# Optimization experiments

Measured on AMD Instinct MI355X. Metric: run time of the kernel, lower is better.

## Reference

```python
import jax, jax.numpy as jnp
import numpy as np

N_NODES = 100000
D_IN = 128
D_OUT = 128
N_EDGES = 50000
EDGE_SIZE = 16  # nodes per hyperedge (assumed unique within an edge)


def setup_inputs() -> dict:
    key = jax.random.key(0)
    ks = jax.random.split(key, 8)
    # hypergraph in flat membership (CSR-like) form
    member_nodes = jax.random.randint(ks[0], (N_EDGES * EDGE_SIZE,), 0, N_NODES)
    edge_ids = jnp.repeat(jnp.arange(N_EDGES), EDGE_SIZE)
    H = jax.random.normal(ks[1], (N_NODES, D_IN), dtype=jnp.float32)
    input_weight = jax.random.uniform(ks[2], (N_NODES, 2), dtype=jnp.float32)
    std = 1.0 / np.sqrt(D_OUT)
    W = jax.random.uniform(ks[3], (D_IN, D_OUT), minval=-std, maxval=std, dtype=jnp.float32)
    bias = jax.random.uniform(ks[4], (D_OUT,), minval=-std, maxval=std, dtype=jnp.float32)

    def lin(k, fan_in, fan_out):
        b = 1.0 / np.sqrt(fan_in)
        k1, k2 = jax.random.split(k)
        w = jax.random.uniform(k1, (fan_in, fan_out), minval=-b, maxval=b, dtype=jnp.float32)
        bb = jax.random.uniform(k2, (fan_out,), minval=-b, maxval=b, dtype=jnp.float32)
        return w, bb

    fc1_w, fc1_b = lin(ks[5], 2, 10)
    fc2_w, fc2_b = lin(ks[6], 10, 5)
    fc3_w, fc3_b = lin(ks[7], 5, 1)
    return {
        "member_nodes": member_nodes, "edge_ids": edge_ids,
        "H": H, "input_weight": input_weight,
        "W": W, "bias": bias,
        "fc1_w": fc1_w, "fc1_b": fc1_b,
        "fc2_w": fc2_w, "fc2_b": fc2_b,
        "fc3_w": fc3_w, "fc3_b": fc3_b,
    }


def reference(member_nodes, edge_ids, H, input_weight, W, bias,
              fc1_w, fc1_b, fc2_w, fc2_b, fc3_w, fc3_b):
    # Weight_net (eval mode -> dropout is identity): per-node scalar weight in (0,1)
    h1 = jax.nn.relu(input_weight @ fc1_w + fc1_b)
    h2 = jax.nn.relu(h1 @ fc2_w + fc2_b)
    W2 = jax.nn.sigmoid(h2 @ fc3_w + fc3_b)  # [N, 1]

    # signal_shift_hypergraph_: per-edge weighted sum, broadcast, scatter-add
    HW2 = H * W2                                   # [N, d]
    gathered = HW2[member_nodes]                   # [M, d]
    edge_sum = jax.ops.segment_sum(gathered, edge_ids, num_segments=N_EDGES)   # [E, d]
    edge_size = jax.ops.segment_sum(jnp.ones((member_nodes.shape[0],), H.dtype),
                                    edge_ids, num_segments=N_EDGES)            # [E]
    contrib = (edge_sum[edge_ids] - H[member_nodes]) / (edge_size[edge_ids] - 1.0)[:, None]
    new_signal = H + jax.ops.segment_sum(contrib, member_nodes, num_segments=N_NODES)

    # row-normalize (1/rowsum with inf -> 0)
    rowsum = new_signal.sum(axis=1)
    r_inv = jnp.where(rowsum != 0, 1.0 / rowsum, 0.0)
    AH = new_signal * r_inv[:, None]

    return AH @ W + bias
```

## Files before the change

### kernel.cpp

```cpp
#include <hip/hip_runtime.h>
#include <math.h>

#define EDGE_SZ 16
#define CAP 32

typedef __attribute__((ext_vector_type(8))) short bf16x8;
typedef __attribute__((ext_vector_type(4))) float f32x4;

__device__ __forceinline__ unsigned short f2bf(float x) {
    unsigned u = __builtin_bit_cast(unsigned, x);
    unsigned r = (u + 0x7fff + ((u >> 16) & 1)) >> 16;
    return (unsigned short)r;
}
__device__ __forceinline__ unsigned pack2bf(float lo, float hi) {
    return ((unsigned)f2bf(hi) << 16) | (unsigned)f2bf(lo);
}
__device__ __forceinline__ float bf_lo(unsigned u) {
    return __builtin_bit_cast(float, u << 16);
}
__device__ __forceinline__ float bf_hi(unsigned u) {
    return __builtin_bit_cast(float, u & 0xffff0000u);
}

__global__ __launch_bounds__(256) void prep_kernel(
    const float* __restrict__ H, const float* __restrict__ iw,
    const float* __restrict__ fc1_w, const float* __restrict__ fc1_b,
    const float* __restrict__ fc2_w, const float* __restrict__ fc2_b,
    const float* __restrict__ fc3_w, const float* __restrict__ fc3_b,
    unsigned* __restrict__ Hwb, float* __restrict__ Hs, float* __restrict__ Hws,
    int* __restrict__ cursor, int n)
{
    int wave = __builtin_amdgcn_readfirstlane(
        blockIdx.x * (blockDim.x >> 6) + (threadIdx.x >> 6));
    int lane = threadIdx.x & 63;
    if (wave >= n) return;
    float xx = iw[wave * 2 + 0], xy = iw[wave * 2 + 1];
    float h1[10];
#pragma unroll
    for (int j = 0; j < 10; ++j) {
        float v = xx * fc1_w[j] + xy * fc1_w[10 + j] + fc1_b[j];
        h1[j] = v > 0.f ? v : 0.f;
    }
    float h2[5];
#pragma unroll
    for (int j = 0; j < 5; ++j) {
        float v = fc2_b[j];
#pragma unroll
        for (int k = 0; k < 10; ++k) v += h1[k] * fc2_w[k * 5 + j];
        h2[j] = v > 0.f ? v : 0.f;
    }
    float z = fc3_b[0];
#pragma unroll
    for (int j = 0; j < 5; ++j) z += h2[j] * fc3_w[j];
    float w2v = 1.f / (1.f + expf(-z));

    float2 h = ((const float2*)H)[wave * 64 + lane];
    Hwb[wave * 64 + lane] = pack2bf(h.x * w2v, h.y * w2v);
    float part = h.x + h.y;
#pragma unroll
    for (int off = 32; off >= 1; off >>= 1) part += __shfl_xor(part, off, 64);
    if (lane == 0) { Hs[wave] = part; Hws[wave] = part * w2v; cursor[wave] = 0; }
}

__global__ __launch_bounds__(256) void wt_kernel(
    const float* __restrict__ W, unsigned short* __restrict__ Wtg)
{
    int i = blockIdx.x * blockDim.x + threadIdx.x;
    int n = i >> 7, k = i & 127;
    Wtg[i] = f2bf(W[k * 128 + n]);
}

__global__ void fill_kernel(const int* __restrict__ mn, int* __restrict__ cursor,
                            unsigned short* __restrict__ bucket, int m)
{
    int i = blockIdx.x * blockDim.x + threadIdx.x;
    if (i < m) {
        int node = mn[i];
        int pos = atomicAdd(&cursor[node], 1);
        if (pos < CAP)
            bucket[node * CAP + pos] = (unsigned short)(i >> 4);
    }
}

__global__ __launch_bounds__(256) void edge_sum_kernel(
    const int* __restrict__ mn, const unsigned* __restrict__ Hwb,
    const float* __restrict__ Hws, unsigned* __restrict__ esb,
    float* __restrict__ Se, int E)
{
    int pair = __builtin_amdgcn_readfirstlane(
        blockIdx.x * (blockDim.x >> 6) + (threadIdx.x >> 6));
    int lane = threadIdx.x & 63;
    int e0 = pair * 2;
    if (e0 >= E) return;
    int e1 = e0 + 1;
    int n0[EDGE_SZ], n1[EDGE_SZ];
#pragma unroll
    for (int m = 0; m < EDGE_SZ; ++m) n0[m] = mn[e0 * EDGE_SZ + m];
#pragma unroll
    for (int m = 0; m < EDGE_SZ; ++m) n1[m] = mn[e1 * EDGE_SZ + m];
    unsigned u0[EDGE_SZ], u1[EDGE_SZ];
#pragma unroll
    for (int m = 0; m < EDGE_SZ; ++m) u0[m] = Hwb[n0[m] * 64 + lane];
#pragma unroll
    for (int m = 0; m < EDGE_SZ; ++m) u1[m] = Hwb[n1[m] * 64 + lane];
    float se0 = 0.f, se1 = 0.f;
#pragma unroll
    for (int m = 0; m < EDGE_SZ; ++m) { se0 += Hws[n0[m]]; se1 += Hws[n1[m]]; }
    float ax0 = 0.f, ay0 = 0.f, ax1 = 0.f, ay1 = 0.f;
#pragma unroll
    for (int m = 0; m < EDGE_SZ; ++m) {
        ax0 += bf_lo(u0[m]); ay0 += bf_hi(u0[m]);
        ax1 += bf_lo(u1[m]); ay1 += bf_hi(u1[m]);
    }
    esb[e0 * 64 + lane] = pack2bf(ax0, ay0);
    esb[e1 * 64 + lane] = pack2bf(ax1, ay1);
    if (lane == 0) { Se[e0] = se0; Se[e1] = se1; }
}

__global__ __launch_bounds__(256) void node_update_kernel(
    const float* __restrict__ H, const unsigned* __restrict__ esb,
    const float* __restrict__ Hs, const float* __restrict__ Se,
    const int* __restrict__ cursor, const unsigned short* __restrict__ bucket,
    unsigned* __restrict__ AHb, int n, int E)
{
    int pair = __builtin_amdgcn_readfirstlane(
        blockIdx.x * (blockDim.x >> 6) + (threadIdx.x >> 6));
    int lane = threadIdx.x & 63;
    int n0 = pair * 2;
    if (n0 >= n) return;
    int n1 = n0 + 1;
    float2 h0 = ((const float2*)H)[n0 * 64 + lane];
    float2 h1 = ((const float2*)H)[n1 * 64 + lane];
    int d0 = cursor[n0]; if (d0 > CAP) d0 = CAP;
    int d1 = cursor[n1]; if (d1 > CAP) d1 = CAP;
    const unsigned* b0 = (const unsigned*)(bucket + (size_t)n0 * CAP);
    const unsigned* b1 = (const unsigned*)(bucket + (size_t)n1 * CAP);
    float ax0 = 0.f, ay0 = 0.f, ss0 = 0.f;
    float ax1 = 0.f, ay1 = 0.f, ss1 = 0.f;
    int dm = d0 > d1 ? d0 : d1;
    for (int k0 = 0; k0 < dm; k0 += 8) {
        int e0[8], e1[8];
#pragma unroll
        for (int j = 0; j < 8; ++j) {
            unsigned dw0 = b0[(k0 >> 1) + (j >> 1)];
            unsigned dw1 = b1[(k0 >> 1) + (j >> 1)];
            unsigned ev0 = (j & 1) ? (dw0 >> 16) : (dw0 & 0xffffu);
            unsigned ev1 = (j & 1) ? (dw1 >> 16) : (dw1 & 0xffffu);
            e0[j] = ev0 < (unsigned)E ? (int)ev0 : 0;
            e1[j] = ev1 < (unsigned)E ? (int)ev1 : 0;
        }
        unsigned v0[8], v1[8];
#pragma unroll
        for (int j = 0; j < 8; ++j) v0[j] = esb[e0[j] * 64 + lane];
#pragma unroll
        for (int j = 0; j < 8; ++j) v1[j] = esb[e1[j] * 64 + lane];
        float s0[8], s1[8];
#pragma unroll
        for (int j = 0; j < 8; ++j) { s0[j] = Se[e0[j]]; s1[j] = Se[e1[j]]; }
#pragma unroll
        for (int j = 0; j < 8; ++j) {
            bool p0 = (k0 + j < d0), p1 = (k0 + j < d1);
            ax0 += p0 ? bf_lo(v0[j]) : 0.f;
            ay0 += p0 ? bf_hi(v0[j]) : 0.f;
            ss0 += p0 ? s0[j] : 0.f;
            ax1 += p1 ? bf_lo(v1[j]) : 0.f;
            ay1 += p1 ? bf_hi(v1[j]) : 0.f;
            ss1 += p1 ? s1[j] : 0.f;
        }
    }
    const float inv15 = 1.f / 15.f;
    float sc0 = 1.f - (float)d0 * inv15;
    float sc1 = 1.f - (float)d1 * inv15;
    float nx0 = h0.x * sc0 + ax0 * inv15, ny0 = h0.y * sc0 + ay0 * inv15;
    float nx1 = h1.x * sc1 + ax1 * inv15, ny1 = h1.y * sc1 + ay1 * inv15;
    float s0t = Hs[n0] * sc0 + ss0 * inv15;
    float s1t = Hs[n1] * sc1 + ss1 * inv15;
    float ri0 = (s0t != 0.f) ? 1.f / s0t : 0.f;
    float ri1 = (s1t != 0.f) ? 1.f / s1t : 0.f;
    AHb[n0 * 64 + lane] = pack2bf(nx0 * ri0, ny0 * ri0);
    AHb[n1 * 64 + lane] = pack2bf(nx1 * ri1, ny1 * ri1);
}

#define WT_LD 136
__global__ __launch_bounds__(256) void gemm_kernel(
    const unsigned short* __restrict__ AHb, const unsigned short* __restrict__ Wtg,
    const float* __restrict__ bias, float* __restrict__ out, int M)
{
    __shared__ short Wt[128 * WT_LD];
    int t = threadIdx.x;
    for (int i = t; i < 8192; i += 256) {
        unsigned dw = ((const unsigned*)Wtg)[i];
        int n = i >> 6, k2 = i & 63;
        *(unsigned*)&Wt[n * WT_LD + k2 * 2] = dw;
    }
    __syncthreads();

    int lane = t & 63;
    int m16 = lane & 15;
    int quad = lane >> 4;
    int wrow0 = blockIdx.x * 64 + (t >> 6) * 16;

    int arow = wrow0 + m16;
    if (arow >= M) arow = M - 1;

    f32x4 acc[8] = {};
#pragma unroll
    for (int kc = 0; kc < 4; ++kc) {
        int k0 = kc * 32;
        bf16x8 a = *(const bf16x8*)&AHb[arow * 128 + k0 + quad * 8];
#pragma unroll
        for (int ct = 0; ct < 8; ++ct) {
            bf16x8 b = *(const bf16x8*)&Wt[(ct * 16 + m16) * WT_LD + k0 + quad * 8];
            acc[ct] = __builtin_amdgcn_mfma_f32_16x16x32_bf16(a, b, acc[ct], 0, 0, 0);
        }
    }

#pragma unroll
    for (int ct = 0; ct < 8; ++ct) {
        float bv = bias[ct * 16 + m16];
#pragma unroll
        for (int r = 0; r < 4; ++r) {
            int row = wrow0 + quad * 4 + r;
            if (row < M)
                out[row * 128 + ct * 16 + m16] = acc[ct][r] + bv;
        }
    }
}

extern "C" void kernel_launch(void* const* d_in, const int* in_sizes, int n_in,
                              void* d_out, int out_size, void* d_ws, size_t ws_size,
                              hipStream_t stream)
{
    const int*   mn   = (const int*)d_in[0];
    const float* H    = (const float*)d_in[2];
    const float* iw   = (const float*)d_in[3];
    const float* W    = (const float*)d_in[4];
    const float* bias = (const float*)d_in[5];
    const float* fc1w = (const float*)d_in[6];
    const float* fc1b = (const float*)d_in[7];
    const float* fc2w = (const float*)d_in[8];
    const float* fc2b = (const float*)d_in[9];
    const float* fc3w = (const float*)d_in[10];
    const float* fc3b = (const float*)d_in[11];
    float* out = (float*)d_out;

    const int M = in_sizes[0];
    const int E = M / EDGE_SZ;
    const int N = in_sizes[2] / 128;

    char* ws = (char*)d_ws;
    size_t off = 0;
    auto alloc = [&](size_t bytes) -> char* {
        char* p = ws + off;
        off = (off + bytes + 15) & ~(size_t)15;
        return p;
    };
    unsigned*       Hwb    = (unsigned*)alloc((size_t)N * 64 * 4);
    float*          Hs     = (float*)alloc((size_t)N * 4);
    float*          Hws    = (float*)alloc((size_t)N * 4);
    unsigned*       esb    = (unsigned*)alloc((size_t)E * 64 * 4);
    float*          Se     = (float*)alloc((size_t)E * 4);
    unsigned*       AHb    = (unsigned*)alloc((size_t)N * 64 * 4);
    int*            cursor = (int*)alloc((size_t)N * 4);
    unsigned short* bucket = (unsigned short*)alloc((size_t)N * CAP * 2);
    unsigned short* Wtg    = (unsigned short*)alloc((size_t)128 * 128 * 2);
    (void)ws_size;

    prep_kernel<<<(N + 3) / 4, 256, 0, stream>>>(
        H, iw, fc1w, fc1b, fc2w, fc2b, fc3w, fc3b, Hwb, Hs, Hws, cursor, N);
    wt_kernel<<<64, 256, 0, stream>>>(W, Wtg);
    fill_kernel<<<(M + 255) / 256, 256, 0, stream>>>(mn, cursor, bucket, M);
    edge_sum_kernel<<<(E / 2 + 3) / 4, 256, 0, stream>>>(mn, Hwb, Hws, esb, Se, E);
    node_update_kernel<<<(N / 2 + 3) / 4, 256, 0, stream>>>(
        H, esb, Hs, Se, cursor, bucket, AHb, N, E);
    gemm_kernel<<<(N + 63) / 64, 256, 0, stream>>>(
        (const unsigned short*)AHb, Wtg, bias, out, N);
}
```

Baseline: 278.3 us.

## Merge prep and fill kernels, move cursor reset to init, batch four nodes per wave

Folds the weight transpose and the cursor zeroing into a small init kernel. Runs the bucket fill and the per-node prep as disjoint block ranges of a single launch, which cuts the launch count and lets the two independent workloads overlap. The node update kernel now handles four nodes per wave instead of two, issuing more independent gathers per loop iteration to hide latency. The cost is more register pressure, and more lanes sit idle on padding when the nodes in a group have uneven degrees.

```diff
diff --git a/kernel.cpp b/kernel.cpp
--- a/kernel.cpp
+++ b/kernel.cpp
@@ -22,16 +22,40 @@
     return __builtin_bit_cast(float, u & 0xffff0000u);
 }
 
-__global__ __launch_bounds__(256) void prep_kernel(
+__global__ __launch_bounds__(256) void init_kernel(
+    const float* __restrict__ W, unsigned short* __restrict__ Wtg,
+    int* __restrict__ cursor, int n)
+{
+    int i = blockIdx.x * blockDim.x + threadIdx.x;
+    if (i < n) cursor[i] = 0;
+    if (i < 16384) {
+        int nn = i >> 7, k = i & 127;
+        Wtg[i] = f2bf(W[k * 128 + nn]);
+    }
+}
+
+__global__ __launch_bounds__(256) void prep_fill_kernel(
     const float* __restrict__ H, const float* __restrict__ iw,
     const float* __restrict__ fc1_w, const float* __restrict__ fc1_b,
     const float* __restrict__ fc2_w, const float* __restrict__ fc2_b,
     const float* __restrict__ fc3_w, const float* __restrict__ fc3_b,
     unsigned* __restrict__ Hwb, float* __restrict__ Hs, float* __restrict__ Hws,
-    int* __restrict__ cursor, int n)
-{
+    const int* __restrict__ mn, int* __restrict__ cursor,
+    unsigned short* __restrict__ bucket,
+    int n, int m, int fill_blocks)
+{
+    if ((int)blockIdx.x < fill_blocks) {
+        int i = blockIdx.x * blockDim.x + threadIdx.x;
+        if (i < m) {
+            int node = mn[i];
+            int pos = atomicAdd(&cursor[node], 1);
+            if (pos < CAP)
+                bucket[node * CAP + pos] = (unsigned short)(i >> 4);
+        }
+        return;
+    }
     int wave = __builtin_amdgcn_readfirstlane(
-        blockIdx.x * (blockDim.x >> 6) + (threadIdx.x >> 6));
+        (blockIdx.x - fill_blocks) * (blockDim.x >> 6) + (threadIdx.x >> 6));
     int lane = threadIdx.x & 63;
     if (wave >= n) return;
     float xx = iw[wave * 2 + 0], xy = iw[wave * 2 + 1];
@@ -59,27 +83,7 @@
     float part = h.x + h.y;
 #pragma unroll
     for (int off = 32; off >= 1; off >>= 1) part += __shfl_xor(part, off, 64);
-    if (lane == 0) { Hs[wave] = part; Hws[wave] = part * w2v; cursor[wave] = 0; }
-}
-
-__global__ __launch_bounds__(256) void wt_kernel(
-    const float* __restrict__ W, unsigned short* __restrict__ Wtg)
-{
-    int i = blockIdx.x * blockDim.x + threadIdx.x;
-    int n = i >> 7, k = i & 127;
-    Wtg[i] = f2bf(W[k * 128 + n]);
-}
-
-__global__ void fill_kernel(const int* __restrict__ mn, int* __restrict__ cursor,
-                            unsigned short* __restrict__ bucket, int m)
-{
-    int i = blockIdx.x * blockDim.x + threadIdx.x;
-    if (i < m) {
-        int node = mn[i];
-        int pos = atomicAdd(&cursor[node], 1);
-        if (pos < CAP)
-            bucket[node * CAP + pos] = (unsigned short)(i >> 4);
-    }
+    if (lane == 0) { Hs[wave] = part; Hws[wave] = part * w2v; }
 }
 
 __global__ __launch_bounds__(256) void edge_sum_kernel(
@@ -123,62 +127,69 @@
     const int* __restrict__ cursor, const unsigned short* __restrict__ bucket,
     unsigned* __restrict__ AHb, int n, int E)
 {
-    int pair = __builtin_amdgcn_readfirstlane(
+    int grp = __builtin_amdgcn_readfirstlane(
         blockIdx.x * (blockDim.x >> 6) + (threadIdx.x >> 6));
     int lane = threadIdx.x & 63;
-    int n0 = pair * 2;
-    if (n0 >= n) return;
-    int n1 = n0 + 1;
-    float2 h0 = ((const float2*)H)[n0 * 64 + lane];
-    float2 h1 = ((const float2*)H)[n1 * 64 + lane];
-    int d0 = cursor[n0]; if (d0 > CAP) d0 = CAP;
-    int d1 = cursor[n1]; if (d1 > CAP) d1 = CAP;
-    const unsigned* b0 = (const unsigned*)(bucket + (size_t)n0 * CAP);
-    const unsigned* b1 = (const unsigned*)(bucket + (size_t)n1 * CAP);
-    float ax0 = 0.f, ay0 = 0.f, ss0 = 0.f;
-    float ax1 = 0.f, ay1 = 0.f, ss1 = 0.f;
-    int dm = d0 > d1 ? d0 : d1;
+    int base = grp * 4;
+    if (base >= n) return;
+    float2 h[4];
+    int d[4];
+    const unsigned* bp[4];
+    float ax[4], ay[4], ss[4];
+    int dm = 0;
+#pragma unroll
+    for (int q = 0; q < 4; ++q) {
+        int nq = base + q; if (nq >= n) nq = n - 1;
+        h[q] = ((const float2*)H)[nq * 64 + lane];
+        int dq = cursor[nq]; if (dq > CAP) dq = CAP;
+        if (base + q >= n) dq = 0;
+        d[q] = dq;
+        if (dq > dm) dm = dq;
+        bp[q] = (const unsigned*)(bucket + (size_t)nq * CAP);
+        ax[q] = 0.f; ay[q] = 0.f; ss[q] = 0.f;
+    }
     for (int k0 = 0; k0 < dm; k0 += 8) {
-        int e0[8], e1[8];
-#pragma unroll
-        for (int j = 0; j < 8; ++j) {
-            unsigned dw0 = b0[(k0 >> 1) + (j >> 1)];
-            unsigned dw1 = b1[(k0 >> 1) + (j >> 1)];
-            unsigned ev0 = (j & 1) ? (dw0 >> 16) : (dw0 & 0xffffu);
-            unsigned ev1 = (j & 1) ? (dw1 >> 16) : (dw1 & 0xffffu);
-            e0[j] = ev0 < (unsigned)E ? (int)ev0 : 0;
-            e1[j] = ev1 < (unsigned)E ? (int)ev1 : 0;
-        }
-        unsigned v0[8], v1[8];
-#pragma unroll
-        for (int j = 0; j < 8; ++j) v0[j] = esb[e0[j] * 64 + lane];
-#pragma unroll
-        for (int j = 0; j < 8; ++j) v1[j] = esb[e1[j] * 64 + lane];
-        float s0[8], s1[8];
-#pragma unroll
-        for (int j = 0; j < 8; ++j) { s0[j] = Se[e0[j]]; s1[j] = Se[e1[j]]; }
-#pragma unroll
-        for (int j = 0; j < 8; ++j) {
-            bool p0 = (k0 + j < d0), p1 = (k0 + j < d1);
-            ax0 += p0 ? bf_lo(v0[j]) : 0.f;
-            ay0 += p0 ? bf_hi(v0[j]) : 0.f;
-            ss0 += p0 ? s0[j] : 0.f;
-            ax1 += p1 ? bf_lo(v1[j]) : 0.f;
-            ay1 += p1 ? bf_hi(v1[j]) : 0.f;
-            ss1 += p1 ? s1[j] : 0.f;
-        }
+        int e[4][8];
+#pragma unroll
+        for (int q = 0; q < 4; ++q)
+#pragma unroll
+            for (int j = 0; j < 8; ++j) {
+                unsigned dw = bp[q][(k0 >> 1) + (j >> 1)];
+                unsigned ev = (j & 1) ? (dw >> 16) : (dw & 0xffffu);
+                e[q][j] = ev < (unsigned)E ? (int)ev : 0;
+            }
+        unsigned v[4][8];
+#pragma unroll
+        for (int q = 0; q < 4; ++q)
+#pragma unroll
+            for (int j = 0; j < 8; ++j) v[q][j] = esb[e[q][j] * 64 + lane];
+        float s[4][8];
+#pragma unroll
+        for (int q = 0; q < 4; ++q)
+#pragma unroll
+            for (int j = 0; j < 8; ++j) s[q][j] = Se[e[q][j]];
+#pragma unroll
+        for (int q = 0; q < 4; ++q)
+#pragma unroll
+            for (int j = 0; j < 8; ++j) {
+                bool p = (k0 + j < d[q]);
+                ax[q] += p ? bf_lo(v[q][j]) : 0.f;
+                ay[q] += p ? bf_hi(v[q][j]) : 0.f;
+                ss[q] += p ? s[q][j] : 0.f;
+            }
     }
     const float inv15 = 1.f / 15.f;
-    float sc0 = 1.f - (float)d0 * inv15;
-    float sc1 = 1.f - (float)d1 * inv15;
-    float nx0 = h0.x * sc0 + ax0 * inv15, ny0 = h0.y * sc0 + ay0 * inv15;
-    float nx1 = h1.x * sc1 + ax1 * inv15, ny1 = h1.y * sc1 + ay1 * inv15;
-    float s0t = Hs[n0] * sc0 + ss0 * inv15;
-    float s1t = Hs[n1] * sc1 + ss1 * inv15;
-    float ri0 = (s0t != 0.f) ? 1.f / s0t : 0.f;
-    float ri1 = (s1t != 0.f) ? 1.f / s1t : 0.f;
-    AHb[n0 * 64 + lane] = pack2bf(nx0 * ri0, ny0 * ri0);
-    AHb[n1 * 64 + lane] = pack2bf(nx1 * ri1, ny1 * ri1);
+#pragma unroll
+    for (int q = 0; q < 4; ++q) {
+        if (base + q >= n) break;
+        int nq = base + q;
+        float sc = 1.f - (float)d[q] * inv15;
+        float nx = h[q].x * sc + ax[q] * inv15;
+        float ny = h[q].y * sc + ay[q] * inv15;
+        float st = Hs[nq] * sc + ss[q] * inv15;
+        float ri = (st != 0.f) ? 1.f / st : 0.f;
+        AHb[nq * 64 + lane] = pack2bf(nx * ri, ny * ri);
+    }
 }
 
 #define WT_LD 136
@@ -266,12 +277,15 @@
     unsigned short* Wtg    = (unsigned short*)alloc((size_t)128 * 128 * 2);
     (void)ws_size;
 
-    prep_kernel<<<(N + 3) / 4, 256, 0, stream>>>(
-        H, iw, fc1w, fc1b, fc2w, fc2b, fc3w, fc3b, Hwb, Hs, Hws, cursor, N);
-    wt_kernel<<<64, 256, 0, stream>>>(W, Wtg);
-    fill_kernel<<<(M + 255) / 256, 256, 0, stream>>>(mn, cursor, bucket, M);
+    const int fill_blocks = (M + 255) / 256;
+    const int prep_blocks = (N + 3) / 4;
+
+    init_kernel<<<(N + 255) / 256, 256, 0, stream>>>(W, Wtg, cursor, N);
+    prep_fill_kernel<<<fill_blocks + prep_blocks, 256, 0, stream>>>(
+        H, iw, fc1w, fc1b, fc2w, fc2b, fc3w, fc3b,
+        Hwb, Hs, Hws, mn, cursor, bucket, N, M, fill_blocks);
     edge_sum_kernel<<<(E / 2 + 3) / 4, 256, 0, stream>>>(mn, Hwb, Hws, esb, Se, E);
-    node_update_kernel<<<(N / 2 + 3) / 4, 256, 0, stream>>>(
+    node_update_kernel<<<((N + 3) / 4 + 3) / 4, 256, 0, stream>>>(
         H, esb, Hs, Se, cursor, bucket, AHb, N, E);
     gemm_kernel<<<(N + 63) / 64, 256, 0, stream>>>(
         (const unsigned short*)AHb, Wtg, bias, out, N);
```

Result: slower. 290.3 us (+4.3%).
